# Kernel optimization log

Measured on AMD Instinct MI355X. Metric: run time of the kernel, lower is better.

## Reference

```python
import jax, jax.numpy as jnp
import numpy as np

B, M, K, KNN = 2, 256, 64, 16
CXYZ, CFEAT = 3, 61
CIN = CXYZ + CFEAT  # 64
MLPS = [64, 128]
SUMM = sum(MLPS)    # 192
CALIB = 64
EXP = [256, 512]
OUT = 256
EPS = 1e-5


def bn(x, g, b):
    # BatchNorm eval mode with running_mean=0, running_var=1 (channel axis 1)
    shape = (1, -1) + (1,) * (x.ndim - 2)
    return x * (g / jnp.sqrt(1.0 + EPS)).reshape(shape) + b.reshape(shape)


def knn(x, k):
    xx = jnp.sum(x * x, axis=1)                      # (B, N)
    inner = jnp.einsum('bcn,bcm->bnm', x, x)         # (B, N, N)
    pd = 2.0 * inner - xx[:, :, None] - xx[:, None, :]
    return jax.lax.top_k(pd, k)[1]                   # (B, N, k)


def graph_feature(x, idx):
    # x: (B, C, N), idx: (B, N, k) -> (B, 2C, N, k)
    xt = jnp.transpose(x, (0, 2, 1))                 # (B, N, C)
    nb = jax.vmap(lambda a, i: a[i])(xt, idx)        # (B, N, k, C)
    ctr = xt[:, :, None, :]
    feat = jnp.concatenate([nb - ctr, jnp.broadcast_to(ctr, nb.shape)], axis=-1)
    return jnp.transpose(feat, (0, 3, 1, 2))


def forward(xyz, feats, e1_w, e1_g, e1_b, e2_w, e2_g, e2_b,
            cal1_w, cal1_g, cal1_b, cal2_w, cal2_bias,
            exp1_w, exp1_g, exp1_b, exp2_w, exp2_g, exp2_b,
            red_w, red_g, red_b, sc1_w, sc1_b, sc2_w, sc2_b,
            sc_n1_g, sc_n1_b, sc_n2_g, sc_n2_b):
    x3 = xyz.reshape(B * M, K, CXYZ).transpose(0, 2, 1)      # (BM, 3, K)
    f = feats.reshape(B * M, K, CFEAT).transpose(0, 2, 1)    # (BM, 61, K)
    idx = knn(x3, KNN)                                        # USE_FEATS_DIS=False: knn once on xyz
    x = jnp.concatenate([x3, f], axis=1)                      # (BM, 64, K)
    outs = []
    for W, g, b in ((e1_w, e1_g, e1_b), (e2_w, e2_g, e2_b)):
        gf = graph_feature(x, idx)                            # (BM, 2C, K, knn)
        y = jax.nn.relu(bn(jnp.einsum('oc,bcnk->bonk', W, gf), g, b))
        x = y.max(axis=-1)                                    # (BM, mlp_i, K)
        outs.append(x)
    x = jnp.concatenate(outs, axis=1)                         # (BM, 192, K)
    c = jax.nn.relu(bn(jnp.einsum('oc,bcn->bon', cal1_w, x), cal1_g, cal1_b))
    c = jnp.einsum('oc,bcn->bon', cal2_w, c) + cal2_bias[None, :, None]
    x = jax.nn.sigmoid(c) * x
    x = jax.nn.relu(bn(jnp.einsum('oc,bcn->bon', exp1_w, x), exp1_g, exp1_b))
    x = jax.nn.relu(bn(jnp.einsum('oc,bcn->bon', exp2_w, x), exp2_g, exp2_b))
    x = x.max(axis=-1).reshape(B, M, EXP[1]).transpose(0, 2, 1)  # (B, 512, M)
    x = jax.nn.relu(bn(jnp.einsum('oc,bcm->bom', red_w, x), red_g, red_b))
    x = bn(x + x, sc_n1_g, sc_n1_b)
    h = jax.nn.relu(jnp.einsum('oc,bcm->bom', sc1_w, x) + sc1_b[None, :, None])
    h = jnp.einsum('oc,bcm->bom', sc2_w, h) + sc2_b[None, :, None]
    x = bn(x + h, sc_n2_g, sc_n2_b)
    return x                                                  # (B, 256, M)


def setup_inputs() -> dict:
    key = jax.random.key(0)
    ks = jax.random.split(key, 16)
    w = lambda k, s: jax.random.normal(k, s, jnp.float32) * 0.05
    ones = lambda n: jnp.ones((n,), jnp.float32)
    zeros = lambda n: jnp.zeros((n,), jnp.float32)
    return {
        'xyz': jax.random.normal(ks[0], (B, M, K, CXYZ), jnp.float32),
        'feats': jax.random.normal(ks[1], (B, M, K, CFEAT), jnp.float32),
        'e1_w': w(ks[2], (MLPS[0], 2 * CIN)), 'e1_g': ones(MLPS[0]), 'e1_b': zeros(MLPS[0]),
        'e2_w': w(ks[3], (MLPS[1], 2 * MLPS[0])), 'e2_g': ones(MLPS[1]), 'e2_b': zeros(MLPS[1]),
        'cal1_w': w(ks[4], (CALIB, SUMM)), 'cal1_g': ones(CALIB), 'cal1_b': zeros(CALIB),
        'cal2_w': w(ks[5], (SUMM, CALIB)), 'cal2_bias': zeros(SUMM),
        'exp1_w': w(ks[6], (EXP[0], SUMM)), 'exp1_g': ones(EXP[0]), 'exp1_b': zeros(EXP[0]),
        'exp2_w': w(ks[7], (EXP[1], EXP[0])), 'exp2_g': ones(EXP[1]), 'exp2_b': zeros(EXP[1]),
        'red_w': w(ks[8], (OUT, EXP[1])), 'red_g': ones(OUT), 'red_b': zeros(OUT),
        'sc1_w': w(ks[9], (OUT, OUT)), 'sc1_b': zeros(OUT),
        'sc2_w': w(ks[10], (OUT, OUT)), 'sc2_b': zeros(OUT),
        'sc_n1_g': ones(OUT), 'sc_n1_b': zeros(OUT),
        'sc_n2_g': ones(OUT), 'sc_n2_b': zeros(OUT),
    }


def reference(xyz, feats, e1_w, e1_g, e1_b, e2_w, e2_g, e2_b,
              cal1_w, cal1_g, cal1_b, cal2_w, cal2_bias,
              exp1_w, exp1_g, exp1_b, exp2_w, exp2_g, exp2_b,
              red_w, red_g, red_b, sc1_w, sc1_b, sc2_w, sc2_b,
              sc_n1_g, sc_n1_b, sc_n2_g, sc_n2_b):
    return forward(xyz, feats, e1_w, e1_g, e1_b, e2_w, e2_g, e2_b,
                   cal1_w, cal1_g, cal1_b, cal2_w, cal2_bias,
                   exp1_w, exp1_g, exp1_b, exp2_w, exp2_g, exp2_b,
                   red_w, red_g, red_b, sc1_w, sc1_b, sc2_w, sc2_b,
                   sc_n1_g, sc_n1_b, sc_n2_g, sc_n2_b)
```

## Files before the change

kernel.cpp:

```cpp
#include <hip/hip_runtime.h>
#include <hip/hip_bf16.h>
#include <math.h>
#include <stddef.h>

#define DEV __device__ __forceinline__
__device__ const float BNS = 0.99999500003749968f;

typedef __bf16 bf16x8 __attribute__((ext_vector_type(8)));
typedef float  f32x4  __attribute__((ext_vector_type(4)));

DEV unsigned short f2bs(float v){
  union{ __hip_bfloat16 b; unsigned short u; } c; c.b=__float2bfloat16(v); return c.u;
}
DEV float bs2f(unsigned short u){
  union{ unsigned short u; __hip_bfloat16 b; } c; c.u=u; return __bfloat162float(c.b);
}


__global__ __launch_bounds__(256) void k_prep(const float* __restrict__ e1_w,
    const float* __restrict__ e2_w, const float* __restrict__ cal1_w,
    const float* __restrict__ cal2_w, const float* __restrict__ exp1_w,
    const float* __restrict__ exp2_w, unsigned short* __restrict__ Whi,
    unsigned short* __restrict__ Wlo,
    const float* __restrict__ red_w, const float* __restrict__ sc1_w,
    const float* __restrict__ sc2_w, float* __restrict__ Wt_red,
    float* __restrict__ Wt_s1, float* __restrict__ Wt_s2){
  __shared__ float s[32][33];
  int bid = blockIdx.x;
  if(bid < 896){
    const float* src; unsigned short *hi,*lo; int mode, O=0, i0;
    if(bid<32)      { src=e1_w;  hi=Whi;       lo=Wlo;       mode=1; O= 64; i0=bid*256; }
    else if(bid<96) { src=e2_w;  hi=Whi+8192;  lo=Wlo+8192;  mode=1; O=128; i0=(bid-32)*256; }
    else if(bid<144){ src=cal1_w;hi=Whi+24576; lo=Wlo+24576; mode=0;        i0=(bid-96)*256; }
    else if(bid<192){ src=cal2_w;hi=Whi+36864; lo=Wlo+36864; mode=0;        i0=(bid-144)*256; }
    else if(bid<384){ src=exp1_w;hi=Whi+49152; lo=Wlo+49152; mode=0;        i0=(bid-192)*256; }
    else            { src=exp2_w;hi=Whi+98304; lo=Wlo+98304; mode=0;        i0=(bid-384)*256; }
    int i = i0 + threadIdx.x;
    float v;
    if(mode==0) v = src[i];
    else {
      int row=i>>6, c=i&63;
      v = (row<O) ? src[row*128+c] : (src[(row-O)*128+64+c]-src[(row-O)*128+c]);
    }
    unsigned short h=f2bs(v); hi[i]=h; lo[i]=f2bs(v-bs2f(h));
  } else {
    int lb = bid-896;
    const float* in; float* out; int O,K;
    if(lb<128){ in=red_w; out=Wt_red; O=256; K=512; }
    else if(lb<192){ in=sc1_w; out=Wt_s1; O=256; K=256; lb-=128; }
    else { in=sc2_w; out=Wt_s2; O=256; K=256; lb-=192; }
    int nt=O>>5;
    int to=lb%nt, tk=lb/nt;
    int c=threadIdx.x&31, r8=threadIdx.x>>5;
    #pragma unroll
    for(int p=0;p<4;p++){
      int r=r8+p*8;
      s[r][c]=in[(size_t)(to*32+r)*K + tk*32 + c];
    }
    __syncthreads();
    #pragma unroll
    for(int p=0;p<4;p++){
      int r=r8+p*8;
      out[(size_t)(tk*32+r)*O + to*32 + c]=s[c][r];
    }
  }
}

__global__ __launch_bounds__(256) void k_knne1(const float* __restrict__ xyz,
    const float* __restrict__ feats,
    const unsigned short* __restrict__ Wh, const unsigned short* __restrict__ Wl,
    int* __restrict__ idxo, const float* __restrict__ gg,
    const float* __restrict__ bb, unsigned short* __restrict__ cat){
  __shared__ float bufA[64*65];
  __shared__ float bufB[64*65];
  __shared__ __align__(16) unsigned short sb[64*136];
  __shared__ int   ips[64*16];
  __shared__ float sx0[64], sx1[64], sx2[64], sxx[64];
  __shared__ float cv[64][4];
  __shared__ int   ci[64][4];
  int bm = blockIdx.x;
  int tid = threadIdx.x, n = tid&63, s = tid>>6;
  int wid = tid>>6, lane = tid&63;
  int l15 = lane&15, q = lane>>4;
  if(s==0){
    const float* xp = xyz + (size_t)(bm*64+n)*3;
    float px=xp[0], py=xp[1], pz=xp[2];
    sx0[n]=px; sx1[n]=py; sx2[n]=pz; sxx[n]=px*px+py*py+pz*pz;
  }
  __syncthreads();
  {
    float px=sx0[n], py=sx1[n], pz=sx2[n], xxn=sxx[n];
    #pragma unroll
    for(int t=0;t<16;t++){
      int m = s*16+t;
      float inner = px*sx0[m]+py*sx1[m]+pz*sx2[m];
      bufA[n*65+m] = 2.0f*inner - xxn - sxx[m];
    }
  }
  __syncthreads();
  for(int j=0;j<16;j++){
    float best=-3.4e38f; int bi=s*16;
    #pragma unroll
    for(int t=0;t<16;t++){ int m=s*16+t; float v=bufA[n*65+m]; if(v>best){best=v;bi=m;} }
    cv[n][s]=best; ci[n][s]=bi;
    __syncthreads();
    if(s==0){
      float bb2=cv[n][0]; int bj=ci[n][0];
      #pragma unroll
      for(int q2=1;q2<4;q2++){ if(cv[n][q2]>bb2){bb2=cv[n][q2]; bj=ci[n][q2];} }
      ips[n*16+j]=bj; bufA[n*65+bj]=-3.4e38f;
    }
    __syncthreads();
  }
  #pragma unroll
  for(int t=0;t<4;t++) idxo[bm*1024 + tid*4 + t] = ips[tid*4 + t];
  {
    unsigned short* r = sb + n*136;
    if(s==0){
      float px=sx0[n], py=sx1[n], pz=sx2[n];
      unsigned short h;
      h=f2bs(px); r[0]=h; r[64]=f2bs(px-bs2f(h));
      h=f2bs(py); r[1]=h; r[65]=f2bs(py-bs2f(h));
      h=f2bs(pz); r[2]=h; r[66]=f2bs(pz-bs2f(h));
    }
    const float* fp = feats + (size_t)(bm*64+n)*61;
    #pragma unroll
    for(int t=0;t<16;t++){
      int cc = s*16+t;
      if(cc<61){
        float v=fp[cc]; unsigned short h=f2bs(v);
        r[3+cc]=h; r[64+3+cc]=f2bs(v-bs2f(h));
      }
    }
  }
  __syncthreads();
  int rbase = ((wid<2)?0:64) + (wid&1)*32;
  f32x4 acc[2][4];
  #pragma unroll
  for(int a=0;a<2;a++)
    #pragma unroll
    for(int d=0;d<4;d++) acc[a][d]=(f32x4){0.f,0.f,0.f,0.f};
  #pragma unroll
  for(int kc=0;kc<2;kc++){
    int k0=kc*32;
    size_t a0=(size_t)(rbase+l15)*64 + k0 + q*8;
    size_t a1=(size_t)(rbase+16+l15)*64 + k0 + q*8;
    bf16x8 a0h=*(const bf16x8*)(Wh+a0), a0l=*(const bf16x8*)(Wl+a0);
    bf16x8 a1h=*(const bf16x8*)(Wh+a1), a1l=*(const bf16x8*)(Wl+a1);
    #pragma unroll
    for(int nt=0;nt<4;nt++){
      int row = nt*16 + l15;
      bf16x8 bh = *(const bf16x8*)&sb[row*136 + k0 + q*8];
      bf16x8 bl = *(const bf16x8*)&sb[row*136 + 64 + k0 + q*8];
      acc[0][nt]=__builtin_amdgcn_mfma_f32_16x16x32_bf16(a0h,bh,acc[0][nt],0,0,0);
      acc[0][nt]=__builtin_amdgcn_mfma_f32_16x16x32_bf16(a0h,bl,acc[0][nt],0,0,0);
      acc[0][nt]=__builtin_amdgcn_mfma_f32_16x16x32_bf16(a0l,bh,acc[0][nt],0,0,0);
      acc[1][nt]=__builtin_amdgcn_mfma_f32_16x16x32_bf16(a1h,bh,acc[1][nt],0,0,0);
      acc[1][nt]=__builtin_amdgcn_mfma_f32_16x16x32_bf16(a1h,bl,acc[1][nt],0,0,0);
      acc[1][nt]=__builtin_amdgcn_mfma_f32_16x16x32_bf16(a1l,bh,acc[1][nt],0,0,0);
    }
  }
  __syncthreads();
  {
    float* dst = (wid<2)? bufA : bufB;
    int ro = (wid&1)*32;
    #pragma unroll
    for(int mt=0;mt<2;mt++)
      #pragma unroll
      for(int nt=0;nt<4;nt++)
        #pragma unroll
        for(int rr=0;rr<4;rr++)
          dst[(ro+mt*16+q*4+rr)*65 + nt*16+l15] = acc[mt][nt][rr];
  }
  __syncthreads();
  {
    int o = lane;
    float sc = gg[o]*BNS, bi = bb[o];
    #pragma unroll 4
    for(int j=0;j<16;j++){
      int nn = wid*16 + j;
      const int* ip = &ips[nn*16];
      float mz = -3.4e38f;
      #pragma unroll
      for(int k=0;k<16;k++) mz = fmaxf(mz, bufA[o*65 + ip[k]]);
      float v = fmaxf(sc*(mz + bufB[o*65 + nn]) + bi, 0.f);
      unsigned short hv = f2bs(v);
      size_t cb = ((size_t)bm*64+nn)*384 + o;
      cat[cb] = hv; cat[cb+192] = f2bs(v - bs2f(hv));
    }
  }
}

template<int O>
__global__ __launch_bounds__(256) void k_edge2(
    const unsigned short* __restrict__ Wh, const unsigned short* __restrict__ Wl,
    const unsigned short* __restrict__ X, int RS, int LO,
    const int* __restrict__ idxg, const float* __restrict__ gg,
    const float* __restrict__ bb, unsigned short* __restrict__ cat, int coloff){
  __shared__ float zs[64*65];
  __shared__ float ds[64*65];
  int bm = blockIdx.x;
  int tid = threadIdx.x, wid = tid>>6, lane = tid&63;
  int l15 = lane&15, q = lane>>4;
  const int* ip0 = idxg + bm*1024;
  size_t xrow = ((size_t)bm*64 + l15)*RS;
  for(int ch=0; ch<O/64; ch++){
    int rbase = ((wid<2)?0:O) + ch*64 + (wid&1)*32;
    f32x4 acc[2][4];
    #pragma unroll
    for(int a=0;a<2;a++)
      #pragma unroll
      for(int d=0;d<4;d++) acc[a][d]=(f32x4){0.f,0.f,0.f,0.f};
    #pragma unroll
    for(int kc=0;kc<2;kc++){
      int k0=kc*32;
      size_t a0=(size_t)(rbase+l15)*64 + k0 + q*8;
      size_t a1=(size_t)(rbase+16+l15)*64 + k0 + q*8;
      bf16x8 a0h=*(const bf16x8*)(Wh+a0), a0l=*(const bf16x8*)(Wl+a0);
      bf16x8 a1h=*(const bf16x8*)(Wh+a1), a1l=*(const bf16x8*)(Wl+a1);
      #pragma unroll
      for(int nt=0;nt<4;nt++){
        const unsigned short* xp = X + xrow + (size_t)nt*16*RS + k0 + q*8;
        bf16x8 bh=*(const bf16x8*)xp, bl=*(const bf16x8*)(xp+LO);
        acc[0][nt]=__builtin_amdgcn_mfma_f32_16x16x32_bf16(a0h,bh,acc[0][nt],0,0,0);
        acc[0][nt]=__builtin_amdgcn_mfma_f32_16x16x32_bf16(a0h,bl,acc[0][nt],0,0,0);
        acc[0][nt]=__builtin_amdgcn_mfma_f32_16x16x32_bf16(a0l,bh,acc[0][nt],0,0,0);
        acc[1][nt]=__builtin_amdgcn_mfma_f32_16x16x32_bf16(a1h,bh,acc[1][nt],0,0,0);
        acc[1][nt]=__builtin_amdgcn_mfma_f32_16x16x32_bf16(a1h,bl,acc[1][nt],0,0,0);
        acc[1][nt]=__builtin_amdgcn_mfma_f32_16x16x32_bf16(a1l,bh,acc[1][nt],0,0,0);
      }
    }
    __syncthreads();
    float* dst = (wid<2)? zs : ds;
    int ro = (wid&1)*32;
    #pragma unroll
    for(int mt=0;mt<2;mt++)
      #pragma unroll
      for(int nt=0;nt<4;nt++)
        #pragma unroll
        for(int rr=0;rr<4;rr++)
          dst[(ro+mt*16+q*4+rr)*65 + nt*16+l15] = acc[mt][nt][rr];
    __syncthreads();
    int o = ch*64 + lane;
    float s = gg[o]*BNS, bi = bb[o];
    #pragma unroll 4
    for(int j=0;j<16;j++){
      int n = wid*16 + j;
      const int* ip = ip0 + n*16;
      float mz = -3.4e38f;
      #pragma unroll
      for(int k=0;k<16;k++) mz = fmaxf(mz, zs[lane*65 + ip[k]]);
      float v = fmaxf(s*(mz + ds[lane*65 + n]) + bi, 0.f);
      unsigned short hv = f2bs(v);
      size_t cb = ((size_t)bm*64+n)*384 + coloff + o;
      cat[cb] = hv; cat[cb+192] = f2bs(v - bs2f(hv));
    }
    __syncthreads();
  }
}

__global__ __launch_bounds__(256) void k_cal(
    const unsigned short* __restrict__ Whi, const unsigned short* __restrict__ Wlo,
    unsigned short* __restrict__ cats,
    const float* __restrict__ c1g, const float* __restrict__ c1b,
    const float* __restrict__ c2bias){
  const unsigned short* c1w_h = Whi+24576; const unsigned short* c1w_l = Wlo+24576;
  const unsigned short* c2w_h = Whi+36864; const unsigned short* c2w_l = Wlo+36864;
  __shared__ __align__(16) unsigned short sW[64*64];
  __shared__ __align__(16) unsigned short sX[128*64];
  __shared__ __align__(16) unsigned short c1L[128*136];
  int rt = blockIdx.x;
  int tid = threadIdx.x, wid = tid>>6, lane = tid&63;
  int l15 = lane&15, q = lane>>4;
  f32x4 acc1[8];
  #pragma unroll
  for(int d=0;d<8;d++) acc1[d]=(f32x4){0.f,0.f,0.f,0.f};
  size_t xbase = (size_t)rt*128*384;
  for(int kc=0;kc<6;kc++){
    int k0=kc*32;
    __syncthreads();
    #pragma unroll
    for(int i=0;i<2;i++){
      int U = tid + i*256;
      int r = U>>3, up = U&7, u = up ^ (r&7);
      const unsigned short* src = (u<4)
        ? (c1w_h + (size_t)r*192 + k0 + u*8)
        : (c1w_l + (size_t)r*192 + k0 + (u-4)*8);
      *(uint4*)&sW[U*8] = *(const uint4*)src;
    }
    #pragma unroll
    for(int i=0;i<4;i++){
      int U = tid + i*256;
      int r = U>>3, up = U&7, u = up ^ (r&7);
      const unsigned short* src = cats + xbase + (size_t)r*384
        + (u<4 ? (size_t)(k0 + u*8) : (size_t)(192 + k0 + (u-4)*8));
      *(uint4*)&sX[U*8] = *(const uint4*)src;
    }
    __syncthreads();
    int o = wid*16 + l15;
    bf16x8 wh = *(const bf16x8*)&sW[(o*8 + ((  q) ^ (o&7)))*8];
    bf16x8 wl = *(const bf16x8*)&sW[(o*8 + ((4+q) ^ (o&7)))*8];
    #pragma unroll
    for(int nf=0;nf<8;nf++){
      int r = nf*16 + l15;
      bf16x8 xh = *(const bf16x8*)&sX[(r*8 + ((  q) ^ (r&7)))*8];
      bf16x8 xl = *(const bf16x8*)&sX[(r*8 + ((4+q) ^ (r&7)))*8];
      acc1[nf]=__builtin_amdgcn_mfma_f32_16x16x32_bf16(wh,xh,acc1[nf],0,0,0);
      acc1[nf]=__builtin_amdgcn_mfma_f32_16x16x32_bf16(wh,xl,acc1[nf],0,0,0);
      acc1[nf]=__builtin_amdgcn_mfma_f32_16x16x32_bf16(wl,xh,acc1[nf],0,0,0);
    }
  }
  {
    int ob0 = wid*16 + q*4;
    float s0[4], b0[4];
    #pragma unroll
    for(int r=0;r<4;r++){ s0[r]=c1g[ob0+r]*BNS; b0[r]=c1b[ob0+r]; }
    #pragma unroll
    for(int nf=0;nf<8;nf++){
      int n = nf*16 + l15;
      unsigned short hv[4], lv[4];
      #pragma unroll
      for(int r=0;r<4;r++){
        float v = fmaxf(acc1[nf][r]*s0[r]+b0[r], 0.f);
        hv[r]=f2bs(v); lv[r]=f2bs(v - bs2f(hv[r]));
      }
      *(ushort4*)&c1L[n*136 + ob0]      = make_ushort4(hv[0],hv[1],hv[2],hv[3]);
      *(ushort4*)&c1L[n*136 + 64 + ob0] = make_ushort4(lv[0],lv[1],lv[2],lv[3]);
    }
  }
  __syncthreads();
  f32x4 acc2[3][8];
  #pragma unroll
  for(int a=0;a<3;a++)
    #pragma unroll
    for(int d=0;d<8;d++) acc2[a][d]=(f32x4){0.f,0.f,0.f,0.f};
  #pragma unroll
  for(int kc=0;kc<2;kc++){
    int k0=kc*32;
    bf16x8 ah[3], al[3];
    #pragma unroll
    for(int mt=0;mt<3;mt++){
      int o = wid*48 + mt*16 + l15;
      ah[mt]=*(const bf16x8*)(c2w_h + (size_t)o*64 + k0 + q*8);
      al[mt]=*(const bf16x8*)(c2w_l + (size_t)o*64 + k0 + q*8);
    }
    #pragma unroll
    for(int nf=0;nf<8;nf++){
      int n = nf*16 + l15;
      bf16x8 bh = *(const bf16x8*)&c1L[n*136 + k0 + q*8];
      bf16x8 bl = *(const bf16x8*)&c1L[n*136 + 64 + k0 + q*8];
      #pragma unroll
      for(int mt=0;mt<3;mt++){
        acc2[mt][nf]=__builtin_amdgcn_mfma_f32_16x16x32_bf16(ah[mt],bh,acc2[mt][nf],0,0,0);
        acc2[mt][nf]=__builtin_amdgcn_mfma_f32_16x16x32_bf16(ah[mt],bl,acc2[mt][nf],0,0,0);
        acc2[mt][nf]=__builtin_amdgcn_mfma_f32_16x16x32_bf16(al[mt],bh,acc2[mt][nf],0,0,0);
      }
    }
  }
  #pragma unroll
  for(int mt=0;mt<3;mt++){
    int ob0 = wid*48 + mt*16 + q*4;
    float bi[4];
    #pragma unroll
    for(int r=0;r<4;r++) bi[r]=c2bias[ob0+r];
    #pragma unroll
    for(int nf=0;nf<8;nf++){
      size_t row = (size_t)rt*128 + nf*16 + l15;
      size_t rb = row*384;
      ushort4 hv = *(ushort4*)(cats + rb + ob0);
      ushort4 lv = *(ushort4*)(cats + rb + 192 + ob0);
      unsigned short h[4]={hv.x,hv.y,hv.z,hv.w}, l[4]={lv.x,lv.y,lv.z,lv.w};
      #pragma unroll
      for(int r=0;r<4;r++){
        float g = 1.f/(1.f+__expf(-(acc2[mt][nf][r]+bi[r])));
        float f = (bs2f(h[r])+bs2f(l[r]))*g;
        h[r]=f2bs(f); l[r]=f2bs(f-bs2f(h[r]));
      }
      *(ushort4*)(cats + rb + ob0)       = make_ushort4(h[0],h[1],h[2],h[3]);
      *(ushort4*)(cats + rb + 192 + ob0) = make_ushort4(l[0],l[1],l[2],l[3]);
    }
  }
}

template<int K, int BO, int EPI>
__global__ __launch_bounds__(256) void k_mm2(
    const unsigned short* __restrict__ Whi, const unsigned short* __restrict__ Wlo,
    const unsigned short* __restrict__ X, void* __restrict__ Og,
    const float* __restrict__ sg, const float* __restrict__ bg, int O){
  constexpr int WO = BO/4;
  constexpr int MT = WO/16;
  constexpr int WUNITS = BO*8;
  __shared__ __align__(16) unsigned short sW[BO*64];
  __shared__ __align__(16) unsigned short sX[128*64];
  int rt = blockIdx.x;
  int o0 = blockIdx.y*BO;
  int tid = threadIdx.x, wid = tid>>6, lane = tid&63;
  int l15 = lane&15, q = lane>>4;
  f32x4 acc[MT][8];
  #pragma unroll
  for(int a=0;a<MT;a++)
    #pragma unroll
    for(int d=0;d<8;d++) acc[a][d]=(f32x4){0.f,0.f,0.f,0.f};
  size_t xbase = (size_t)rt*128*2*K;
  for(int kc=0; kc<K/32; kc++){
    int k0 = kc*32;
    __syncthreads();
    #pragma unroll
    for(int i=0;i<WUNITS/256;i++){
      int U = tid + i*256;
      int r = U>>3, up = U&7, u = up ^ (r&7);
      const unsigned short* src = (u<4)
        ? (Whi + (size_t)(o0+r)*K + k0 + u*8)
        : (Wlo + (size_t)(o0+r)*K + k0 + (u-4)*8);
      *(uint4*)&sW[U*8] = *(const uint4*)src;
    }
    #pragma unroll
    for(int i=0;i<4;i++){
      int U = tid + i*256;
      int r = U>>3, up = U&7, u = up ^ (r&7);
      const unsigned short* src = X + xbase + (size_t)r*2*K
        + (u<4 ? (size_t)(k0 + u*8) : (size_t)(K + k0 + (u-4)*8));
      *(uint4*)&sX[U*8] = *(const uint4*)src;
    }
    __syncthreads();
    bf16x8 wf[MT][2];
    #pragma unroll
    for(int mt=0;mt<MT;mt++){
      int o = wid*WO + mt*16 + l15;
      wf[mt][0] = *(const bf16x8*)&sW[(o*8 + ((  q) ^ (o&7)))*8];
      wf[mt][1] = *(const bf16x8*)&sW[(o*8 + ((4+q) ^ (o&7)))*8];
    }
    #pragma unroll
    for(int nf=0;nf<8;nf++){
      int r = nf*16 + l15;
      bf16x8 xh = *(const bf16x8*)&sX[(r*8 + ((  q) ^ (r&7)))*8];
      bf16x8 xl = *(const bf16x8*)&sX[(r*8 + ((4+q) ^ (r&7)))*8];
      #pragma unroll
      for(int mt=0;mt<MT;mt++){
        acc[mt][nf]=__builtin_amdgcn_mfma_f32_16x16x32_bf16(wf[mt][0],xh,acc[mt][nf],0,0,0);
        acc[mt][nf]=__builtin_amdgcn_mfma_f32_16x16x32_bf16(wf[mt][0],xl,acc[mt][nf],0,0,0);
        acc[mt][nf]=__builtin_amdgcn_mfma_f32_16x16x32_bf16(wf[mt][1],xh,acc[mt][nf],0,0,0);
      }
    }
  }
  if(EPI==0){
    unsigned short* ob = (unsigned short*)Og;
    #pragma unroll
    for(int mt=0;mt<MT;mt++){
      int ob0 = o0 + wid*WO + mt*16 + q*4;
      float s0[4], b0[4];
      #pragma unroll
      for(int r=0;r<4;r++){ s0[r]=sg[ob0+r]*BNS; b0[r]=bg[ob0+r]; }
      #pragma unroll
      for(int nf=0;nf<8;nf++){
        size_t row = (size_t)rt*128 + nf*16 + l15;
        size_t rb = row*2*O;
        unsigned short hv[4], lv[4];
        #pragma unroll
        for(int r=0;r<4;r++){
          float v = fmaxf(acc[mt][nf][r]*s0[r]+b0[r], 0.f);
          hv[r]=f2bs(v); lv[r]=f2bs(v - bs2f(hv[r]));
        }
        *(ushort4*)(ob + rb + ob0)     = make_ushort4(hv[0],hv[1],hv[2],hv[3]);
        *(ushort4*)(ob + rb + O + ob0) = make_ushort4(lv[0],lv[1],lv[2],lv[3]);
      }
    }
  } else {
    float* pool = (float*)Og;
    #pragma unroll
    for(int mt=0;mt<MT;mt++){
      int ob0 = o0 + wid*WO + mt*16 + q*4;
      #pragma unroll
      for(int half=0;half<2;half++){
        int bm = 2*rt + half;
        int b = bm>>8, m = bm&255;
        #pragma unroll
        for(int r=0;r<4;r++){
          float s=sg[ob0+r]*BNS, bi=bg[ob0+r];
          float v = acc[mt][half*4+0][r]*s+bi;
          v = fmaxf(v, acc[mt][half*4+1][r]*s+bi);
          v = fmaxf(v, acc[mt][half*4+2][r]*s+bi);
          v = fmaxf(v, acc[mt][half*4+3][r]*s+bi);
          v = fmaxf(v, 0.f);
          v = fmaxf(v, __shfl_xor(v,1));
          v = fmaxf(v, __shfl_xor(v,2));
          v = fmaxf(v, __shfl_xor(v,4));
          v = fmaxf(v, __shfl_xor(v,8));
          if(l15==0) pool[((size_t)b*512 + ob0+r)*256 + m] = v;
        }
      }
    }
  }
}

template<int EPI>
__global__ __launch_bounds__(256) void k_head(const float* __restrict__ Wt,
    const float* __restrict__ Xg, float* __restrict__ Og,
    const float* __restrict__ p0, const float* __restrict__ p1,
    const float* __restrict__ p2, const float* __restrict__ p3,
    const float* __restrict__ res, int O, int K){
  __shared__ float As[32][64];
  __shared__ float Bs[32][32];
  int not_ = O>>6;
  int g = blockIdx.x / not_, ot = blockIdx.x % not_;
  int b = g>>3, mg = g&7;
  int o0 = ot*64;
  int tid=threadIdx.x, tx=tid&7, ty=tid>>3;
  float acc[2][4];
  #pragma unroll
  for(int a=0;a<2;a++)
    #pragma unroll
    for(int d=0;d<4;d++) acc[a][d]=0.f;
  const float* Xb = Xg + (size_t)b*K*256 + mg*32;
  for(int k0=0;k0<K;k0+=32){
    __syncthreads();
    #pragma unroll
    for(int p=0;p<2;p++){
      int r = p*16 + (tid>>4), c4 = (tid&15)*4;
      *(float4*)&As[r][c4] = *(const float4*)&Wt[(size_t)(k0+r)*O + o0 + c4];
    }
    {
      int r = tid>>3, c4 = (tid&7)*4;
      *(float4*)&Bs[r][c4] = *(const float4*)&Xb[(size_t)(k0+r)*256 + c4];
    }
    __syncthreads();
    #pragma unroll
    for(int k=0;k<32;k++){
      float av[2], bv[4];
      av[0]=As[k][ty*2]; av[1]=As[k][ty*2+1];
      #pragma unroll
      for(int d=0;d<4;d++) bv[d]=Bs[k][tx*4+d];
      #pragma unroll
      for(int a=0;a<2;a++)
        #pragma unroll
        for(int d=0;d<4;d++) acc[a][d]+=av[a]*bv[d];
    }
  }
  int m0 = mg*32 + tx*4;
  #pragma unroll
  for(int a=0;a<2;a++){
    int o=o0+ty*2+a;
    float* orow = Og + ((size_t)b*O + o)*256 + m0;
    float v[4];
    if(EPI==0){
      float s=p0[o]*BNS, bi=p1[o], s1=p2[o]*BNS, b1=p3[o];
      #pragma unroll
      for(int d=0;d<4;d++){ float r=fmaxf(acc[a][d]*s+bi,0.f); v[d]=2.f*r*s1+b1; }
    } else if(EPI==1){
      float bi=p0[o];
      #pragma unroll
      for(int d=0;d<4;d++) v[d]=fmaxf(acc[a][d]+bi,0.f);
    } else {
      float bi=p0[o], s2=p1[o]*BNS, b2=p2[o];
      const float* rr = res + ((size_t)b*O + o)*256 + m0;
      #pragma unroll
      for(int d=0;d<4;d++){ float u=rr[d]+acc[a][d]+bi; v[d]=u*s2+b2; }
    }
    *(float4*)orow = make_float4(v[0],v[1],v[2],v[3]);
  }
}

extern "C" void kernel_launch(void* const* d_in, const int* in_sizes, int n_in,
                              void* d_out, int out_size, void* d_ws, size_t ws_size,
                              hipStream_t stream){
  const float* xyz     =(const float*)d_in[0];
  const float* feats   =(const float*)d_in[1];
  const float* e1_w    =(const float*)d_in[2];
  const float* e1_g    =(const float*)d_in[3];
  const float* e1_b    =(const float*)d_in[4];
  const float* e2_w    =(const float*)d_in[5];
  const float* e2_g    =(const float*)d_in[6];
  const float* e2_b    =(const float*)d_in[7];
  const float* cal1_w  =(const float*)d_in[8];
  const float* cal1_g  =(const float*)d_in[9];
  const float* cal1_b  =(const float*)d_in[10];
  const float* cal2_w  =(const float*)d_in[11];
  const float* cal2_bias=(const float*)d_in[12];
  const float* exp1_w  =(const float*)d_in[13];
  const float* exp1_g  =(const float*)d_in[14];
  const float* exp1_b  =(const float*)d_in[15];
  const float* exp2_w  =(const float*)d_in[16];
  const float* exp2_g  =(const float*)d_in[17];
  const float* exp2_b  =(const float*)d_in[18];
  const float* red_w   =(const float*)d_in[19];
  const float* red_g   =(const float*)d_in[20];
  const float* red_b   =(const float*)d_in[21];
  const float* sc1_w   =(const float*)d_in[22];
  const float* sc1_b   =(const float*)d_in[23];
  const float* sc2_w   =(const float*)d_in[24];
  const float* sc2_b   =(const float*)d_in[25];
  const float* sc_n1_g =(const float*)d_in[26];
  const float* sc_n1_b =(const float*)d_in[27];
  const float* sc_n2_g =(const float*)d_in[28];
  const float* sc_n2_b =(const float*)d_in[29];

  char* wsb=(char*)d_ws;
  int*            idx =(int*)           (wsb);
  unsigned short* cats=(unsigned short*)(wsb + 10485760);
  unsigned short* p1s =(unsigned short*)(wsb + 35651584);
  float*          pool=(float*)         (wsb + 69206016);
  float*          x1  =(float*)         (wsb + 70254592);
  float*          hbuf=(float*)         (wsb + 70778880);
  unsigned short* Whi =(unsigned short*)(wsb + 75497472);
  unsigned short* Wlo =(unsigned short*)(wsb + 76021760);
  float*          Wt_red=(float*)       (wsb + 76546048);
  float*          Wt_s1 =(float*)       (wsb + 77070336);
  float*          Wt_s2 =(float*)       (wsb + 77332480);
  unsigned short* e1e_h=Whi;          unsigned short* e1e_l=Wlo;
  unsigned short* e2e_h=Whi+8192;     unsigned short* e2e_l=Wlo+8192;
  unsigned short* e1w_h=Whi+49152;    unsigned short* e1w_l=Wlo+49152;
  unsigned short* e2w_h=Whi+98304;    unsigned short* e2w_l=Wlo+98304;

  k_prep      <<<1152,256,0,stream>>>(e1_w,e2_w,cal1_w,cal2_w,exp1_w,exp2_w,Whi,Wlo,
                                      red_w,sc1_w,sc2_w,Wt_red,Wt_s1,Wt_s2);
  k_knne1     <<<512,256,0,stream>>>(xyz,feats,e1e_h,e1e_l,idx,e1_g,e1_b,cats);
  k_edge2<128><<<512,256,0,stream>>>(e2e_h,e2e_l,cats,384,192,idx,e2_g,e2_b,cats,64);
  k_cal       <<<256,256,0,stream>>>(Whi,Wlo,cats,cal1_g,cal1_b,cal2_bias);
  k_mm2<192,128,0><<<dim3(256,2),256,0,stream>>>(e1w_h,e1w_l,cats,(void*)p1s,exp1_g,exp1_b,256);
  k_mm2<256,128,2><<<dim3(256,4),256,0,stream>>>(e2w_h,e2w_l,p1s,(void*)pool,exp2_g,exp2_b,512);
  k_head<0>   <<< 64,256,0,stream>>>(Wt_red,pool,x1,  red_g,red_b,sc_n1_g,sc_n1_b,nullptr,256,512);
  k_head<1>   <<< 64,256,0,stream>>>(Wt_s1, x1,  hbuf,sc1_b,nullptr,nullptr,nullptr,nullptr,256,256);
  k_head<2>   <<< 64,256,0,stream>>>(Wt_s2, hbuf,(float*)d_out,sc2_b,sc_n2_g,sc_n2_b,nullptr,x1,256,256);
}
```

Measured before the change: 275.4 us.

## Fuse edge-conv layer 2 into KNN kernel and use register top-k selection

Merges the second edge-conv kernel into the KNN/first-layer kernel. Layer-1 outputs (bf16 hi/lo) now stay in shared memory as layer-2 input, and neighbour indices are read from shared memory instead of global. The KNN top-k selection now keeps distances in registers, with 4 lanes per point combining results by shuffle, replacing the shared-memory scan that needed two block barriers per selected neighbour. The intent is to remove one launch, a global round-trip of the intermediate features, and many syncs, at the cost of higher register and shared-memory pressure in one larger kernel.

```diff
diff --git a/kernel.cpp b/kernel.cpp
--- a/kernel.cpp
+++ b/kernel.cpp
@@ -66,18 +66,18 @@
   }
 }
 
-__global__ __launch_bounds__(256) void k_knne1(const float* __restrict__ xyz,
+__global__ __launch_bounds__(256) void k_knne12(const float* __restrict__ xyz,
     const float* __restrict__ feats,
-    const unsigned short* __restrict__ Wh, const unsigned short* __restrict__ Wl,
-    int* __restrict__ idxo, const float* __restrict__ gg,
-    const float* __restrict__ bb, unsigned short* __restrict__ cat){
+    const unsigned short* __restrict__ W1h, const unsigned short* __restrict__ W1l,
+    const unsigned short* __restrict__ W2h, const unsigned short* __restrict__ W2l,
+    int* __restrict__ idxo, const float* __restrict__ g1, const float* __restrict__ b1,
+    const float* __restrict__ g2, const float* __restrict__ b2,
+    unsigned short* __restrict__ cat){
   __shared__ float bufA[64*65];
   __shared__ float bufB[64*65];
   __shared__ __align__(16) unsigned short sb[64*136];
   __shared__ int   ips[64*16];
   __shared__ float sx0[64], sx1[64], sx2[64], sxx[64];
-  __shared__ float cv[64][4];
-  __shared__ int   ci[64][4];
   int bm = blockIdx.x;
   int tid = threadIdx.x, n = tid&63, s = tid>>6;
   int wid = tid>>6, lane = tid&63;
@@ -89,31 +89,27 @@
   }
   __syncthreads();
   {
-    float px=sx0[n], py=sx1[n], pz=sx2[n], xxn=sxx[n];
+    int p = lane>>2, seg = lane&3;
+    int n1 = wid*16 + p;
+    float px=sx0[n1], py=sx1[n1], pz=sx2[n1], xxn=sxx[n1];
+    float pdr[16];
     #pragma unroll
     for(int t=0;t<16;t++){
-      int m = s*16+t;
-      float inner = px*sx0[m]+py*sx1[m]+pz*sx2[m];
-      bufA[n*65+m] = 2.0f*inner - xxn - sxx[m];
-    }
-  }
-  __syncthreads();
-  for(int j=0;j<16;j++){
-    float best=-3.4e38f; int bi=s*16;
-    #pragma unroll
-    for(int t=0;t<16;t++){ int m=s*16+t; float v=bufA[n*65+m]; if(v>best){best=v;bi=m;} }
-    cv[n][s]=best; ci[n][s]=bi;
-    __syncthreads();
-    if(s==0){
-      float bb2=cv[n][0]; int bj=ci[n][0];
-      #pragma unroll
-      for(int q2=1;q2<4;q2++){ if(cv[n][q2]>bb2){bb2=cv[n][q2]; bj=ci[n][q2];} }
-      ips[n*16+j]=bj; bufA[n*65+bj]=-3.4e38f;
-    }
-    __syncthreads();
-  }
-  #pragma unroll
-  for(int t=0;t<4;t++) idxo[bm*1024 + tid*4 + t] = ips[tid*4 + t];
+      int m = seg*16+t;
+      pdr[t] = 2.f*(px*sx0[m]+py*sx1[m]+pz*sx2[m]) - xxn - sxx[m];
+    }
+    for(int j=0;j<16;j++){
+      float bv=-3.4e38f; int bi=seg*16;
+      #pragma unroll
+      for(int t=0;t<16;t++){ if(pdr[t]>bv){bv=pdr[t]; bi=seg*16+t;} }
+      float ov=__shfl_xor(bv,1); int oi=__shfl_xor(bi,1);
+      if(ov>bv || (ov==bv && oi<bi)){bv=ov;bi=oi;}
+      ov=__shfl_xor(bv,2); oi=__shfl_xor(bi,2);
+      if(ov>bv || (ov==bv && oi<bi)){bv=ov;bi=oi;}
+      if(seg==0) ips[n1*16+j]=bi;
+      if((bi>>4)==seg) pdr[bi&15]=-3.4e38f;
+    }
+  }
   {
     unsigned short* r = sb + n*136;
     if(s==0){
@@ -134,78 +130,10 @@
     }
   }
   __syncthreads();
-  int rbase = ((wid<2)?0:64) + (wid&1)*32;
-  f32x4 acc[2][4];
-  #pragma unroll
-  for(int a=0;a<2;a++)
-    #pragma unroll
-    for(int d=0;d<4;d++) acc[a][d]=(f32x4){0.f,0.f,0.f,0.f};
-  #pragma unroll
-  for(int kc=0;kc<2;kc++){
-    int k0=kc*32;
-    size_t a0=(size_t)(rbase+l15)*64 + k0 + q*8;
-    size_t a1=(size_t)(rbase+16+l15)*64 + k0 + q*8;
-    bf16x8 a0h=*(const bf16x8*)(Wh+a0), a0l=*(const bf16x8*)(Wl+a0);
-    bf16x8 a1h=*(const bf16x8*)(Wh+a1), a1l=*(const bf16x8*)(Wl+a1);
-    #pragma unroll
-    for(int nt=0;nt<4;nt++){
-      int row = nt*16 + l15;
-      bf16x8 bh = *(const bf16x8*)&sb[row*136 + k0 + q*8];
-      bf16x8 bl = *(const bf16x8*)&sb[row*136 + 64 + k0 + q*8];
-      acc[0][nt]=__builtin_amdgcn_mfma_f32_16x16x32_bf16(a0h,bh,acc[0][nt],0,0,0);
-      acc[0][nt]=__builtin_amdgcn_mfma_f32_16x16x32_bf16(a0h,bl,acc[0][nt],0,0,0);
-      acc[0][nt]=__builtin_amdgcn_mfma_f32_16x16x32_bf16(a0l,bh,acc[0][nt],0,0,0);
-      acc[1][nt]=__builtin_amdgcn_mfma_f32_16x16x32_bf16(a1h,bh,acc[1][nt],0,0,0);
-      acc[1][nt]=__builtin_amdgcn_mfma_f32_16x16x32_bf16(a1h,bl,acc[1][nt],0,0,0);
-      acc[1][nt]=__builtin_amdgcn_mfma_f32_16x16x32_bf16(a1l,bh,acc[1][nt],0,0,0);
-    }
-  }
-  __syncthreads();
+  #pragma unroll
+  for(int t=0;t<4;t++) idxo[bm*1024 + tid*4 + t] = ips[tid*4 + t];
   {
-    float* dst = (wid<2)? bufA : bufB;
-    int ro = (wid&1)*32;
-    #pragma unroll
-    for(int mt=0;mt<2;mt++)
-      #pragma unroll
-      for(int nt=0;nt<4;nt++)
-        #pragma unroll
-        for(int rr=0;rr<4;rr++)
-          dst[(ro+mt*16+q*4+rr)*65 + nt*16+l15] = acc[mt][nt][rr];
-  }
-  __syncthreads();
-  {
-    int o = lane;
-    float sc = gg[o]*BNS, bi = bb[o];
-    #pragma unroll 4
-    for(int j=0;j<16;j++){
-      int nn = wid*16 + j;
-      const int* ip = &ips[nn*16];
-      float mz = -3.4e38f;
-      #pragma unroll
-      for(int k=0;k<16;k++) mz = fmaxf(mz, bufA[o*65 + ip[k]]);
-      float v = fmaxf(sc*(mz + bufB[o*65 + nn]) + bi, 0.f);
-      unsigned short hv = f2bs(v);
-      size_t cb = ((size_t)bm*64+nn)*384 + o;
-      cat[cb] = hv; cat[cb+192] = f2bs(v - bs2f(hv));
-    }
-  }
-}
-
-template<int O>
-__global__ __launch_bounds__(256) void k_edge2(
-    const unsigned short* __restrict__ Wh, const unsigned short* __restrict__ Wl,
-    const unsigned short* __restrict__ X, int RS, int LO,
-    const int* __restrict__ idxg, const float* __restrict__ gg,
-    const float* __restrict__ bb, unsigned short* __restrict__ cat, int coloff){
-  __shared__ float zs[64*65];
-  __shared__ float ds[64*65];
-  int bm = blockIdx.x;
-  int tid = threadIdx.x, wid = tid>>6, lane = tid&63;
-  int l15 = lane&15, q = lane>>4;
-  const int* ip0 = idxg + bm*1024;
-  size_t xrow = ((size_t)bm*64 + l15)*RS;
-  for(int ch=0; ch<O/64; ch++){
-    int rbase = ((wid<2)?0:O) + ch*64 + (wid&1)*32;
+    int rbase = ((wid<2)?0:64) + (wid&1)*32;
     f32x4 acc[2][4];
     #pragma unroll
     for(int a=0;a<2;a++)
@@ -216,12 +144,13 @@
       int k0=kc*32;
       size_t a0=(size_t)(rbase+l15)*64 + k0 + q*8;
       size_t a1=(size_t)(rbase+16+l15)*64 + k0 + q*8;
-      bf16x8 a0h=*(const bf16x8*)(Wh+a0), a0l=*(const bf16x8*)(Wl+a0);
-      bf16x8 a1h=*(const bf16x8*)(Wh+a1), a1l=*(const bf16x8*)(Wl+a1);
+      bf16x8 a0h=*(const bf16x8*)(W1h+a0), a0l=*(const bf16x8*)(W1l+a0);
+      bf16x8 a1h=*(const bf16x8*)(W1h+a1), a1l=*(const bf16x8*)(W1l+a1);
       #pragma unroll
       for(int nt=0;nt<4;nt++){
-        const unsigned short* xp = X + xrow + (size_t)nt*16*RS + k0 + q*8;
-        bf16x8 bh=*(const bf16x8*)xp, bl=*(const bf16x8*)(xp+LO);
+        int row = nt*16 + l15;
+        bf16x8 bh = *(const bf16x8*)&sb[row*136 + k0 + q*8];
+        bf16x8 bl = *(const bf16x8*)&sb[row*136 + 64 + k0 + q*8];
         acc[0][nt]=__builtin_amdgcn_mfma_f32_16x16x32_bf16(a0h,bh,acc[0][nt],0,0,0);
         acc[0][nt]=__builtin_amdgcn_mfma_f32_16x16x32_bf16(a0h,bl,acc[0][nt],0,0,0);
         acc[0][nt]=__builtin_amdgcn_mfma_f32_16x16x32_bf16(a0l,bh,acc[0][nt],0,0,0);
@@ -231,7 +160,7 @@
       }
     }
     __syncthreads();
-    float* dst = (wid<2)? zs : ds;
+    float* dst = (wid<2)? bufA : bufB;
     int ro = (wid&1)*32;
     #pragma unroll
     for(int mt=0;mt<2;mt++)
@@ -240,22 +169,78 @@
         #pragma unroll
         for(int rr=0;rr<4;rr++)
           dst[(ro+mt*16+q*4+rr)*65 + nt*16+l15] = acc[mt][nt][rr];
-    __syncthreads();
-    int o = ch*64 + lane;
-    float s = gg[o]*BNS, bi = bb[o];
+  }
+  __syncthreads();
+  {
+    int o = lane;
+    float sc = g1[o]*BNS, bi = b1[o];
     #pragma unroll 4
     for(int j=0;j<16;j++){
-      int n = wid*16 + j;
-      const int* ip = ip0 + n*16;
+      int nn = wid*16 + j;
+      const int* ip = &ips[nn*16];
       float mz = -3.4e38f;
       #pragma unroll
-      for(int k=0;k<16;k++) mz = fmaxf(mz, zs[lane*65 + ip[k]]);
-      float v = fmaxf(s*(mz + ds[lane*65 + n]) + bi, 0.f);
+      for(int k=0;k<16;k++) mz = fmaxf(mz, bufA[o*65 + ip[k]]);
+      float v = fmaxf(sc*(mz + bufB[o*65 + nn]) + bi, 0.f);
+      unsigned short hv = f2bs(v), lv = f2bs(v - bs2f(hv));
+      size_t cb = ((size_t)bm*64+nn)*384 + o;
+      cat[cb] = hv; cat[cb+192] = lv;
+      sb[nn*136 + o] = hv; sb[nn*136 + 64 + o] = lv;
+    }
+  }
+  for(int ch=0; ch<2; ch++){
+    __syncthreads();
+    int rbase = ((wid<2)?0:128) + ch*64 + (wid&1)*32;
+    f32x4 acc[2][4];
+    #pragma unroll
+    for(int a=0;a<2;a++)
+      #pragma unroll
+      for(int d=0;d<4;d++) acc[a][d]=(f32x4){0.f,0.f,0.f,0.f};
+    #pragma unroll
+    for(int kc=0;kc<2;kc++){
+      int k0=kc*32;
+      size_t a0=(size_t)(rbase+l15)*64 + k0 + q*8;
+      size_t a1=(size_t)(rbase+16+l15)*64 + k0 + q*8;
+      bf16x8 a0h=*(const bf16x8*)(W2h+a0), a0l=*(const bf16x8*)(W2l+a0);
+      bf16x8 a1h=*(const bf16x8*)(W2h+a1), a1l=*(const bf16x8*)(W2l+a1);
+      #pragma unroll
+      for(int nt=0;nt<4;nt++){
+        int row = nt*16 + l15;
+        bf16x8 bh = *(const bf16x8*)&sb[row*136 + k0 + q*8];
+        bf16x8 bl = *(const bf16x8*)&sb[row*136 + 64 + k0 + q*8];
+        acc[0][nt]=__builtin_amdgcn_mfma_f32_16x16x32_bf16(a0h,bh,acc[0][nt],0,0,0);
+        acc[0][nt]=__builtin_amdgcn_mfma_f32_16x16x32_bf16(a0h,bl,acc[0][nt],0,0,0);
+        acc[0][nt]=__builtin_amdgcn_mfma_f32_16x16x32_bf16(a0l,bh,acc[0][nt],0,0,0);
+        acc[1][nt]=__builtin_amdgcn_mfma_f32_16x16x32_bf16(a1h,bh,acc[1][nt],0,0,0);
+        acc[1][nt]=__builtin_amdgcn_mfma_f32_16x16x32_bf16(a1h,bl,acc[1][nt],0,0,0);
+        acc[1][nt]=__builtin_amdgcn_mfma_f32_16x16x32_bf16(a1l,bh,acc[1][nt],0,0,0);
+      }
+    }
+    __syncthreads();
+    float* dst = (wid<2)? bufA : bufB;
+    int ro = (wid&1)*32;
+    #pragma unroll
+    for(int mt=0;mt<2;mt++)
+      #pragma unroll
+      for(int nt=0;nt<4;nt++)
+        #pragma unroll
+        for(int rr=0;rr<4;rr++)
+          dst[(ro+mt*16+q*4+rr)*65 + nt*16+l15] = acc[mt][nt][rr];
+    __syncthreads();
+    int o = ch*64 + lane;
+    float sc = g2[o]*BNS, bi = b2[o];
+    #pragma unroll 4
+    for(int j=0;j<16;j++){
+      int nn = wid*16 + j;
+      const int* ip = &ips[nn*16];
+      float mz = -3.4e38f;
+      #pragma unroll
+      for(int k=0;k<16;k++) mz = fmaxf(mz, bufA[lane*65 + ip[k]]);
+      float v = fmaxf(sc*(mz + bufB[lane*65 + nn]) + bi, 0.f);
       unsigned short hv = f2bs(v);
-      size_t cb = ((size_t)bm*64+n)*384 + coloff + o;
+      size_t cb = ((size_t)bm*64+nn)*384 + 64 + o;
       cat[cb] = hv; cat[cb+192] = f2bs(v - bs2f(hv));
     }
-    __syncthreads();
   }
 }
 
@@ -613,8 +598,8 @@
 
   k_prep      <<<1152,256,0,stream>>>(e1_w,e2_w,cal1_w,cal2_w,exp1_w,exp2_w,Whi,Wlo,
                                       red_w,sc1_w,sc2_w,Wt_red,Wt_s1,Wt_s2);
-  k_knne1     <<<512,256,0,stream>>>(xyz,feats,e1e_h,e1e_l,idx,e1_g,e1_b,cats);
-  k_edge2<128><<<512,256,0,stream>>>(e2e_h,e2e_l,cats,384,192,idx,e2_g,e2_b,cats,64);
+  k_knne12    <<<512,256,0,stream>>>(xyz,feats,e1e_h,e1e_l,e2e_h,e2e_l,idx,
+                                     e1_g,e1_b,e2_g,e2_b,cats);
   k_cal       <<<256,256,0,stream>>>(Whi,Wlo,cats,cal1_g,cal1_b,cal2_bias);
   k_mm2<192,128,0><<<dim3(256,2),256,0,stream>>>(e1w_h,e1w_l,cats,(void*)p1s,exp1_g,exp1_b,256);
   k_mm2<256,128,2><<<dim3(256,4),256,0,stream>>>(e2w_h,e2w_l,p1s,(void*)pool,exp2_g,exp2_b,512);
```

New measurement: 267.8 us. 2.7% less time.
